# Performance work log

Hardware: AMD Instinct MI355X
Metric: run time of the kernel (lower is better)

The kernel has to match this reference:

```python
import jax, jax.numpy as jnp
import numpy as np

DS = 8  # downsample_factor


def learned_upflow(flow, mask, ds=DS):
    """Convex-combination upsampling, faithful to Model.learned_upflow.

    flow: (n, 2, h, w)   coarse flow at 1/ds resolution
    mask: (n, 9*ds*ds, h, w)  raw (pre-softmax) convex weights
    returns: (n, 2, ds*h, ds*w)
    """
    n, _, h, w = flow.shape
    # mask.view(n, 1, 9, ds, ds, h, w); softmax over the 9 neighbor taps
    m = mask.reshape(n, 1, 9, ds, ds, h, w)
    m = jax.nn.softmax(m, axis=2)

    # F.unfold(ds*flow, [3,3], padding=1) -> 3x3 neighborhoods, row-major
    # kernel order (dy outer, dx inner), channel-major — matches the
    # subsequent view(n, 2, 9, 1, 1, h, w).
    fp = jnp.pad(ds * flow, ((0, 0), (0, 0), (1, 1), (1, 1)))
    patches = jnp.stack(
        [fp[:, :, dy:dy + h, dx:dx + w] for dy in range(3) for dx in range(3)],
        axis=2,
    )  # (n, 2, 9, h, w)

    up = jnp.sum(m * patches[:, :, :, None, None, :, :], axis=2)  # (n,2,ds,ds,h,w)
    # permute(0,1,4,2,5,3) then reshape -> (n, 2, ds*h, ds*w)
    up = up.transpose(0, 1, 4, 2, 5, 3)
    return up.reshape(n, 2, ds * h, ds * w)


def setup_inputs() -> dict:
    key = jax.random.key(0)
    k1, k2 = jax.random.split(key)
    n, h, w = 4, 136, 240
    flow = jax.random.normal(k1, (n, 2, h, w), dtype=jnp.float32)
    mask = jax.random.normal(k2, (n, 9 * DS * DS, h, w), dtype=jnp.float32)
    return {"flow": flow, "mask": mask}


def reference(flow, mask):
    return learned_upflow(flow, mask)
```

## Files before the change

### kernel.cpp

```cpp
#include <hip/hip_runtime.h>

#define HH 136
#define WW 240
#define HW (HH * WW)
#define DS 8
#define OW (DS * WW)
#define OH (DS * HH)

typedef float vf4 __attribute__((ext_vector_type(4)));

__global__ __launch_bounds__(256, 6) void upflow_kernel(
    const float* __restrict__ flow,
    const float* __restrict__ mask,
    float* __restrict__ out) {
  __shared__ float lm[24][WW];

  int h = blockIdx.x;
  int ni = blockIdx.y;
  int i = ni & 7;
  int n = ni >> 3;
  int tid = threadIdx.x;
  int wid = tid >> 6, lane = tid & 63;
  int px = tid;

  float f0[9], f1[9];
  if (px < WW) {
    const float* fb0 = flow + (size_t)(n * 2 + 0) * HW;
    const float* fb1 = flow + (size_t)(n * 2 + 1) * HW;
#pragma unroll
    for (int dy = 0; dy < 3; ++dy) {
      int hh = h + dy - 1;
      bool rok = (hh >= 0) && (hh < HH);
#pragma unroll
      for (int dx = 0; dx < 3; ++dx) {
        int k = dy * 3 + dx;
        int cc = px + dx - 1;
        bool ok = rok && (cc >= 0) && (cc < WW);
        int idx = hh * WW + cc;
        f0[k] = ok ? 8.0f * fb0[idx] : 0.0f;
        f1[k] = ok ? 8.0f * fb1[idx] : 0.0f;
      }
    }
  }

  const float L2E = 1.4426950408889634f;
  float sj[8], d0j[8], d1j[8];
#pragma unroll
  for (int j = 0; j < 8; ++j) { sj[j] = 0.f; d0j[j] = 0.f; d1j[j] = 0.f; }

  const float* mrow = mask + (size_t)n * 576 * HW + (size_t)h * WW;

#pragma unroll
  for (int chunk = 0; chunk < 3; ++chunk) {
    if (lane < 60) {
#pragma unroll
      for (int it = 0; it < 6; ++it) {
        int rr = wid + it * 4;
        int kk = rr >> 3, j = rr & 7;
        const float* src =
            mrow + (size_t)((chunk * 3 + kk) * 64 + i * 8 + j) * HW + lane * 4;
        vf4 v = *(const vf4*)src;
        *(vf4*)&lm[rr][lane * 4] = v;
      }
    }
    __syncthreads();
    if (px < WW) {
#pragma unroll
      for (int j = 0; j < 8; ++j) {
#pragma unroll
        for (int kk = 0; kk < 3; ++kk) {
          const int k = chunk * 3 + kk;
          float e = exp2f(lm[kk * 8 + j][px] * L2E);
          sj[j] += e;
          d0j[j] += e * f0[k];
          d1j[j] += e * f1[k];
        }
      }
    }
    __syncthreads();
  }

  if (px < WW) {
    float o0[8], o1[8];
#pragma unroll
    for (int j = 0; j < 8; ++j) {
      float r = 1.0f / sj[j];
      o0[j] = d0j[j] * r;
      o1[j] = d1j[j] * r;
    }
    size_t ob0 =
        ((size_t)(n * 2 + 0) * OH + (size_t)(h * 8 + i)) * (size_t)OW + px * 8;
    size_t ob1 = ob0 + (size_t)OH * OW;
    vf4 a = {o0[0], o0[1], o0[2], o0[3]};
    vf4 b = {o0[4], o0[5], o0[6], o0[7]};
    vf4 c = {o1[0], o1[1], o1[2], o1[3]};
    vf4 d = {o1[4], o1[5], o1[6], o1[7]};
    *(vf4*)(out + ob0) = a;
    *(vf4*)(out + ob0 + 4) = b;
    *(vf4*)(out + ob1) = c;
    *(vf4*)(out + ob1 + 4) = d;
  }
}

extern "C" void kernel_launch(void* const* d_in, const int* in_sizes, int n_in,
                              void* d_out, int out_size, void* d_ws, size_t ws_size,
                              hipStream_t stream) {
  const float* flow = (const float*)d_in[0];
  const float* mask = (const float*)d_in[1];
  float* out = (float*)d_out;
  dim3 grid(HH, 32);
  upflow_kernel<<<grid, 256, 0, stream>>>(flow, mask, out);
}
```

Baseline: 76.37 us.

## Prefetch next mask chunk into registers while computing current chunk

Each thread now loads the next chunk of mask rows into registers before computing on the current chunk in shared memory, then writes them to LDS after a barrier. This software pipelining is meant to hide global load latency behind the exp/accumulate work. Occupancy hint is lowered from 6 to 5 waves to leave room for the extra 24 prefetch registers. The output normalization is rewritten inline, which is cosmetic.

```diff
diff --git a/kernel.cpp b/kernel.cpp
--- a/kernel.cpp
+++ b/kernel.cpp
@@ -9,7 +9,7 @@
 
 typedef float vf4 __attribute__((ext_vector_type(4)));
 
-__global__ __launch_bounds__(256, 6) void upflow_kernel(
+__global__ __launch_bounds__(256, 5) void upflow_kernel(
     const float* __restrict__ flow,
     const float* __restrict__ mask,
     float* __restrict__ out) {
@@ -22,6 +22,9 @@
   int tid = threadIdx.x;
   int wid = tid >> 6, lane = tid & 63;
   int px = tid;
+  bool stager = lane < 60;
+
+  const float* mrow = mask + ((size_t)n * 576 + i * 8) * HW + (size_t)h * WW;
 
   float f0[9], f1[9];
   if (px < WW) {
@@ -48,22 +51,33 @@
 #pragma unroll
   for (int j = 0; j < 8; ++j) { sj[j] = 0.f; d0j[j] = 0.f; d1j[j] = 0.f; }
 
-  const float* mrow = mask + (size_t)n * 576 * HW + (size_t)h * WW;
+  vf4 pre[6];
+  if (stager) {
+#pragma unroll
+    for (int it = 0; it < 6; ++it) {
+      int rr = wid + it * 4;
+      int kk = rr >> 3, j = rr & 7;
+      pre[it] = *(const vf4*)(mrow + (size_t)(kk * 64 + j) * HW + lane * 4);
+    }
+#pragma unroll
+    for (int it = 0; it < 6; ++it) {
+      int rr = wid + it * 4;
+      *(vf4*)&lm[rr][lane * 4] = pre[it];
+    }
+  }
+  __syncthreads();
 
 #pragma unroll
   for (int chunk = 0; chunk < 3; ++chunk) {
-    if (lane < 60) {
+    if (chunk < 2 && stager) {
 #pragma unroll
       for (int it = 0; it < 6; ++it) {
         int rr = wid + it * 4;
         int kk = rr >> 3, j = rr & 7;
-        const float* src =
-            mrow + (size_t)((chunk * 3 + kk) * 64 + i * 8 + j) * HW + lane * 4;
-        vf4 v = *(const vf4*)src;
-        *(vf4*)&lm[rr][lane * 4] = v;
+        pre[it] = *(const vf4*)(
+            mrow + (size_t)(((chunk + 1) * 3 + kk) * 64 + j) * HW + lane * 4);
       }
     }
-    __syncthreads();
     if (px < WW) {
 #pragma unroll
       for (int j = 0; j < 8; ++j) {
@@ -77,24 +91,30 @@
         }
       }
     }
-    __syncthreads();
+    if (chunk < 2) {
+      __syncthreads();
+      if (stager) {
+#pragma unroll
+        for (int it = 0; it < 6; ++it) {
+          int rr = wid + it * 4;
+          *(vf4*)&lm[rr][lane * 4] = pre[it];
+        }
+      }
+      __syncthreads();
+    }
   }
 
   if (px < WW) {
-    float o0[8], o1[8];
-#pragma unroll
-    for (int j = 0; j < 8; ++j) {
-      float r = 1.0f / sj[j];
-      o0[j] = d0j[j] * r;
-      o1[j] = d1j[j] * r;
-    }
     size_t ob0 =
         ((size_t)(n * 2 + 0) * OH + (size_t)(h * 8 + i)) * (size_t)OW + px * 8;
     size_t ob1 = ob0 + (size_t)OH * OW;
-    vf4 a = {o0[0], o0[1], o0[2], o0[3]};
-    vf4 b = {o0[4], o0[5], o0[6], o0[7]};
-    vf4 c = {o1[0], o1[1], o1[2], o1[3]};
-    vf4 d = {o1[4], o1[5], o1[6], o1[7]};
+    float r0 = 1.0f / sj[0], r1 = 1.0f / sj[1], r2 = 1.0f / sj[2],
+          r3 = 1.0f / sj[3], r4 = 1.0f / sj[4], r5 = 1.0f / sj[5],
+          r6 = 1.0f / sj[6], r7 = 1.0f / sj[7];
+    vf4 a = {d0j[0] * r0, d0j[1] * r1, d0j[2] * r2, d0j[3] * r3};
+    vf4 b = {d0j[4] * r4, d0j[5] * r5, d0j[6] * r6, d0j[7] * r7};
+    vf4 c = {d1j[0] * r0, d1j[1] * r1, d1j[2] * r2, d1j[3] * r3};
+    vf4 d = {d1j[4] * r4, d1j[5] * r5, d1j[6] * r6, d1j[7] * r7};
     *(vf4*)(out + ob0) = a;
     *(vf4*)(out + ob0 + 4) = b;
     *(vf4*)(out + ob1) = c;
```

After: 85.42 us. 11.9% more time.
